# Optimization experiments

Hardware: AMD Instinct MI355X
Metric: run time of the kernel (lower is better)

Reference implementation:

```python
import jax, jax.numpy as jnp
import numpy as np

DIM = 384
RES = 32
NH = 8
RD = 2
B = 64


def _linear_params(key, out_f, in_f, scale=0.02, bias=True):
    kw, kb = jax.random.split(key)
    W = jax.random.normal(kw, (out_f, in_f), dtype=jnp.float32) * scale
    b = jax.random.normal(kb, (out_f,), dtype=jnp.float32) * scale if bias else None
    return W, b


def setup_inputs() -> dict:
    key = jax.random.key(0)
    ks = jax.random.split(key, 16)
    x = jax.random.normal(ks[0], (B, RES, RES, DIM), dtype=jnp.float32)
    Wc_h, bc_h = _linear_params(ks[1], NH * RD, DIM)
    Wg_h, bg_h = _linear_params(ks[2], RES * RES, RES * RD)
    Wo_h, bo_h = _linear_params(ks[3], DIM, DIM)
    Wc_w, bc_w = _linear_params(ks[4], NH * RD, DIM)
    Wg_w, bg_w = _linear_params(ks[5], RES * RES, RES * RD)
    Wo_w, bo_w = _linear_params(ks[6], DIM, DIM)
    Wmlpc, _ = _linear_params(ks[7], DIM, DIM, bias=False)
    Wr1, br1 = _linear_params(ks[8], DIM // 4, DIM)
    Wr2, br2 = _linear_params(ks[9], DIM * 3, DIM // 4)
    Wp, bp = _linear_params(ks[10], DIM, DIM)
    return dict(x=x, Wc_h=Wc_h, bc_h=bc_h, Wg_h=Wg_h, bg_h=bg_h, Wo_h=Wo_h, bo_h=bo_h,
                Wc_w=Wc_w, bc_w=bc_w, Wg_w=Wg_w, bg_w=bg_w, Wo_w=Wo_w, bo_w=bo_w,
                Wmlpc=Wmlpc, Wr1=Wr1, br1=br1, Wr2=Wr2, br2=br2, Wp=Wp, bp=bp)


def _dynamixer_op(x, Wc, bc, Wg, bg, Wo, bo):
    # x: [N, L, C]
    N, L, C = x.shape
    hd = C // NH
    # compress -> [N, L, NH*RD] -> [N, NH, L*RD]
    w = x @ Wc.T + bc
    w = w.reshape(N, L, NH, RD).transpose(0, 2, 1, 3).reshape(N, NH, L * RD)
    # generate -> [N, NH, L, L], softmax over axis -2 (rows)
    w = (w @ Wg.T + bg).reshape(N, NH, L, L)
    w = jax.nn.softmax(w, axis=-2)
    # x -> [N, NH, hd, L]; mix: y[n,h,d,j] = sum_l x[n,h,d,l] * w[n,h,l,j]
    xh = x.reshape(N, L, NH, hd).transpose(0, 2, 3, 1)
    y = jnp.einsum('nhdl,nhlj->nhdj', xh, w)
    y = y.transpose(0, 3, 1, 2).reshape(N, L, C)
    return y @ Wo.T + bo


def reference(x, Wc_h, bc_h, Wg_h, bg_h, Wo_h, bo_h,
              Wc_w, bc_w, Wg_w, bg_w, Wo_w, bo_w,
              Wmlpc, Wr1, br1, Wr2, br2, Wp, bp):
    Bn, H, W, C = x.shape
    # mix along H: batch over (B, W)
    h = _dynamixer_op(x.transpose(0, 2, 1, 3).reshape(Bn * W, H, C),
                      Wc_h, bc_h, Wg_h, bg_h, Wo_h, bo_h)
    h = h.reshape(Bn, W, H, C).transpose(0, 2, 1, 3)
    # mix along W: batch over (B, H)
    w = _dynamixer_op(x.reshape(Bn * H, W, C),
                      Wc_w, bc_w, Wg_w, bg_w, Wo_w, bo_w)
    w = w.reshape(Bn, H, W, C)
    # channel path (no bias)
    c = x @ Wmlpc.T
    # reweighting: global average pool over H, W
    a = (h + w + c).mean(axis=(1, 2))            # [B, C]
    a = jax.nn.gelu(a @ Wr1.T + br1, approximate=False) @ Wr2.T + br2  # [B, 3C]
    a = a.reshape(Bn, C, 3).transpose(2, 0, 1)   # [3, B, C]
    a = jax.nn.softmax(a, axis=0)[:, :, None, None, :]  # [3, B, 1, 1, C]
    out = h * a[0] + w * a[1] + c * a[2]
    return out @ Wp.T + bp
```

## Files before the change

### kernel.cpp

```cpp
#include <hip/hip_runtime.h>

typedef unsigned short u16;
typedef __bf16 bf16_t;
typedef bf16_t bf16x8 __attribute__((ext_vector_type(8)));
typedef float f32x4 __attribute__((ext_vector_type(4)));

__device__ __forceinline__ u16 f2b(float f) {
  union { float f; unsigned u; } v; v.f = f;
  unsigned r = (v.u + 0x7fffu + ((v.u >> 16) & 1u)) >> 16;
  return (u16)r;
}
__device__ __forceinline__ float b2f(u16 b) {
  union { unsigned u; float f; } v; v.u = ((unsigned)b) << 16;
  return v.f;
}
__device__ __forceinline__ f32x4 mfma16(bf16x8 a, bf16x8 b, f32x4 c) {
  return __builtin_amdgcn_mfma_f32_16x16x32_bf16(a, b, c, 0, 0, 0);
}

struct CvtJobs {
  const float* s[8];
  u16* d[8];
  int n[8];
};
__global__ void k0_cvt(CvtJobs j) {
  int job = blockIdx.y;
  const float* s = j.s[job];
  u16* d = j.d[job];
  int n = j.n[job];
  int stride = gridDim.x * blockDim.x * 4;
  for (int i = (blockIdx.x * blockDim.x + threadIdx.x) * 4; i < n; i += stride) {
    float4 v = *(const float4*)(s + i);
    ushort4 o4;
    o4.x = f2b(v.x); o4.y = f2b(v.y); o4.z = f2b(v.z); o4.w = f2b(v.w);
    *(ushort4*)(d + i) = o4;
  }
}

#define LW 392
#define TW 40
#define AW 40

__global__ __launch_bounds__(256, 2) void k1_mixer(
    const float* __restrict__ x,
    const u16* __restrict__ Wc_h_b, const float* __restrict__ bc_h,
    const u16* __restrict__ Wg_h_b, const float* __restrict__ bg_h,
    const u16* __restrict__ Wc_w_b, const float* __restrict__ bc_w,
    const u16* __restrict__ Wg_w_b, const float* __restrict__ bg_w,
    u16* __restrict__ y_h,
    float* __restrict__ psum_yh, float* __restrict__ psum_yw,
    float* __restrict__ psum_x)
{
  __shared__ u16 xs_b[32 * LW];
  __shared__ u16 xs_t[384 * TW];
  __shared__ u16 attn[8 * 32 * AW];
  __shared__ u16 whead[16 * 72];
  __shared__ float rs[8 * 32];

  const int tid = threadIdx.x;
  const int bid = blockIdx.x;
  const int path = bid >> 11;
  const int n = bid & 2047;
  const int b = n >> 5, o = n & 31;
  long base; int strideL;
  if (path == 0) { base = (long)b * 393216 + (long)o * 384;   strideL = 12288; }
  else           { base = (long)b * 393216 + (long)o * 12288; strideL = 384; }
  const float* xseq = x + base;

  const u16* Wc_b = path ? Wc_w_b : Wc_h_b;
  const float* bc = path ? bc_w : bc_h;
  const u16* Wg_b = path ? Wg_w_b : Wg_h_b;
  const float* bg = path ? bg_w : bg_h;

  for (int i = tid; i < 3072; i += 256) {
    int l = i / 96, c4 = (i % 96) * 4;
    float4 v = *(const float4*)(xseq + (long)l * strideL + c4);
    ushort4 w4;
    w4.x = f2b(v.x); w4.y = f2b(v.y); w4.z = f2b(v.z); w4.w = f2b(v.w);
    *(ushort4*)&xs_b[l * LW + c4] = w4;
  }
  for (int i = tid; i < 576; i += 256) whead[576 + i] = 0;
  __syncthreads();

  if (path == 0) {
    for (int i = tid; i < 3072; i += 256) {
      int c = i % 384, l4 = (i / 384) * 4;
      ushort4 w4;
      w4.x = xs_b[(l4 + 0) * LW + c];
      w4.y = xs_b[(l4 + 1) * LW + c];
      w4.z = xs_b[(l4 + 2) * LW + c];
      w4.w = xs_b[(l4 + 3) * LW + c];
      *(ushort4*)&xs_t[c * TW + l4] = w4;
    }
    for (int c = tid; c < 384; c += 256) {
      float s = 0.f;
      for (int l = 0; l < 32; l++) s += b2f(xs_b[l * LW + c]);
      psum_x[(long)n * 384 + c] = s;
    }
  }

  const int wave = tid >> 6, lane = tid & 63;
  const int lq = lane >> 4, lr = lane & 15;
  const f32x4 z = {0.f, 0.f, 0.f, 0.f};

  if (wave < 2) {
    f32x4 acc = z;
    for (int ks = 0; ks < 12; ks++) {
      bf16x8 af  = *(const bf16x8*)&xs_b[(wave * 16 + lr) * LW + ks * 32 + lq * 8];
      bf16x8 bfr = *(const bf16x8*)(Wc_b + lr * 384 + ks * 32 + lq * 8);
      acc = mfma16(af, bfr, acc);
    }
    float bcv = bc[lr];
    for (int r = 0; r < 4; r++) {
      int l = wave * 16 + lq * 4 + r;
      whead[(lr >> 1) * 72 + l * 2 + (lr & 1)] = f2b(acc[r] + bcv);
    }
  }
  __syncthreads();

  {
    bf16x8 ga0 = *(const bf16x8*)&whead[lr * 72 + lq * 8];
    bf16x8 ga1 = *(const bf16x8*)&whead[lr * 72 + 32 + lq * 8];
    for (int t = 0; t < 16; t++) {
      int nt = wave * 16 + t;
      const u16* wg = Wg_b + (nt * 16 + lr) * 64;
      bf16x8 gb0 = *(const bf16x8*)(wg + lq * 8);
      bf16x8 gb1 = *(const bf16x8*)(wg + 32 + lq * 8);
      f32x4 acc = z;
      acc = mfma16(ga0, gb0, acc);
      acc = mfma16(ga1, gb1, acc);
      if (lq < 2) {
        int m = nt * 16 + lr, ii = m >> 5, jj = m & 31;
        for (int r = 0; r < 4; r++)
          attn[((lq * 4 + r) * 32 + jj) * AW + ii] = f2b(acc[r]);
      }
    }
  }
  __syncthreads();

  {
    int h = tid >> 5, j = tid & 31;
    u16* row = &attn[(h * 32 + j) * AW];
    float v[32]; float mx = -1e30f;
    for (int i = 0; i < 32; i++) {
      v[i] = b2f(row[i]) + bg[i * 32 + j];
      mx = fmaxf(mx, v[i]);
    }
    float s = 0.f;
    for (int i = 0; i < 32; i++) { v[i] = __expf(v[i] - mx); s += v[i]; }
    float inv = 1.0f / s;
    for (int i = 0; i < 32; i++) row[i] = f2b(v[i] * inv);
  }
  __syncthreads();

  if (path == 0) {
    for (int hh = 0; hh < 2; hh++) {
      int h = wave * 2 + hh;
      bf16x8 bf0 = *(const bf16x8*)&attn[(h * 32 + lr) * AW + lq * 8];
      bf16x8 bf1 = *(const bf16x8*)&attn[(h * 32 + 16 + lr) * AW + lq * 8];
      for (int mt = 0; mt < 3; mt++) {
        bf16x8 af = *(const bf16x8*)&xs_t[(h * 48 + mt * 16 + lr) * TW + lq * 8];
        f32x4 a0 = mfma16(af, bf0, z);
        f32x4 a1 = mfma16(af, bf1, z);
        for (int r = 0; r < 4; r++) {
          int c = h * 48 + mt * 16 + lq * 4 + r;
          xs_b[lr * LW + c]        = f2b(a0[r]);
          xs_b[(16 + lr) * LW + c] = f2b(a1[r]);
        }
      }
    }
    __syncthreads();
    u16* yout = y_h + base;
    for (int i = tid; i < 1536; i += 256) {
      int l = i / 48, uu = (i % 48) * 8;
      *(uint4*)(yout + (long)l * strideL + uu) = *(const uint4*)&xs_b[l * LW + uu];
    }
    for (int c = tid; c < 384; c += 256) {
      float s = 0.f;
      for (int jj = 0; jj < 32; jj++) s += b2f(xs_b[jj * LW + c]);
      psum_yh[(long)n * 384 + c] = s;
    }
  } else {
    {
      int h = tid >> 5, l = tid & 31;
      float s = 0.f;
      for (int j = 0; j < 32; j++) s += b2f(attn[(h * 32 + j) * AW + l]);
      rs[h * 32 + l] = s;
    }
    __syncthreads();
    for (int c = tid; c < 384; c += 256) {
      int h = c / 48;
      float s = 0.f;
      for (int l = 0; l < 32; l++) s += b2f(xs_b[l * LW + c]) * rs[h * 32 + l];
      psum_yw[(long)n * 384 + c] = s;
    }
  }
}

__global__ __launch_bounds__(384) void k3_scales(
    const float* __restrict__ psum_yh, const float* __restrict__ psum_yw,
    const float* __restrict__ psum_x,
    const float* __restrict__ Wo_h, const float* __restrict__ bo_h,
    const float* __restrict__ Wo_w, const float* __restrict__ bo_w,
    const float* __restrict__ Wmlpc,
    const float* __restrict__ Wr1, const float* __restrict__ br1,
    const float* __restrict__ Wr2, const float* __restrict__ br2,
    float* __restrict__ scal)
{
  __shared__ float ph[384], pw[384], px[384], a[384], r1[96];
  int b = blockIdx.x, t = threadIdx.x;
  float sh = 0.f, sw = 0.f, sx = 0.f;
  for (int o = 0; o < 32; o++) {
    sh += psum_yh[(long)(b * 32 + o) * 384 + t];
    sw += psum_yw[(long)(b * 32 + o) * 384 + t];
    sx += psum_x[(long)(b * 32 + o) * 384 + t];
  }
  ph[t] = sh; pw[t] = sw; px[t] = sx;
  __syncthreads();
  float s1 = 0.f, s2 = 0.f, s3 = 0.f;
  for (int k = 0; k < 384; k++) {
    s1 += ph[k] * Wo_h[t * 384 + k];
    s2 += pw[k] * Wo_w[t * 384 + k];
    s3 += px[k] * Wmlpc[t * 384 + k];
  }
  a[t] = (s1 + s2 + s3) * (1.f / 1024.f) + bo_h[t] + bo_w[t];
  __syncthreads();
  if (t < 96) {
    float s = 0.f;
    for (int k = 0; k < 384; k++) s += a[k] * Wr1[t * 384 + k];
    s += br1[t];
    r1[t] = s * 0.5f * (1.f + erff(s * 0.70710678118654752f));
  }
  __syncthreads();
  {
    float sv[3];
    for (int si = 0; si < 3; si++) {
      float acc = 0.f;
      for (int k = 0; k < 96; k++) acc += r1[k] * Wr2[(t * 3 + si) * 96 + k];
      sv[si] = acc + br2[t * 3 + si];
    }
    float mx = fmaxf(sv[0], fmaxf(sv[1], sv[2]));
    float e0 = __expf(sv[0] - mx), e1 = __expf(sv[1] - mx), e2 = __expf(sv[2] - mx);
    float inv = 1.f / (e0 + e1 + e2);
    scal[0 * 24576 + b * 384 + t] = e0 * inv;
    scal[1 * 24576 + b * 384 + t] = e1 * inv;
    scal[2 * 24576 + b * 384 + t] = e2 * inv;
  }
}

__device__ __forceinline__ void gemm_regB(
    const u16* __restrict__ Bglob, const u16* __restrict__ bufA,
    f32x4 acc[4][6], int wm, int wn, int lq, int lr)
{
  const u16* bp0 = Bglob + (wn * 96 + lr) * 384 + lq * 8;
  const u16* ap0 = bufA + (wm * 64 + lr) * 392 + lq * 8;
  bf16x8 bcur[6], af[4];
#pragma unroll
  for (int nt = 0; nt < 6; nt++) bcur[nt] = *(const bf16x8*)(bp0 + nt * 6144);
#pragma unroll
  for (int mt = 0; mt < 4; mt++) af[mt] = *(const bf16x8*)(ap0 + mt * 6272);
  for (int ks = 0; ks < 12; ks++) {
    bf16x8 bnx[6], an[4];
    const int k1 = (ks < 11) ? (ks + 1) * 32 : 11 * 32;
#pragma unroll
    for (int nt = 0; nt < 6; nt++) bnx[nt] = *(const bf16x8*)(bp0 + nt * 6144 + k1);
#pragma unroll
    for (int mt = 0; mt < 4; mt++) an[mt] = *(const bf16x8*)(ap0 + mt * 6272 + k1);
#pragma unroll
    for (int nt = 0; nt < 6; nt++)
#pragma unroll
      for (int mt = 0; mt < 4; mt++)
        acc[mt][nt] = mfma16(af[mt], bcur[nt], acc[mt][nt]);
#pragma unroll
    for (int nt = 0; nt < 6; nt++) bcur[nt] = bnx[nt];
#pragma unroll
    for (int mt = 0; mt < 4; mt++) af[mt] = an[mt];
  }
}

__global__ __launch_bounds__(512, 2) void k24_final(
    const float* __restrict__ x, const u16* __restrict__ y_h,
    const u16* __restrict__ Wc_w_b, const float* __restrict__ bc_w,
    const u16* __restrict__ Wg_w_b, const float* __restrict__ bg_w,
    const u16* __restrict__ Wo_h_b, const u16* __restrict__ Wo_w_b,
    const u16* __restrict__ Wmlpc_b, const u16* __restrict__ Wp_b,
    const float* __restrict__ bo_h, const float* __restrict__ bo_w,
    const float* __restrict__ bp,
    const float* __restrict__ scal, float* __restrict__ out)
{
  __shared__ u16 bufA[128 * 392];
  __shared__ u16 Bs[384 * 40];
  __shared__ u16 attn[8 * 32 * AW];
  __shared__ u16 whead[16 * 72];

  const int tid = threadIdx.x;
  const int m0 = blockIdx.x * 128;
  const int b = m0 >> 10;
  const int wave = tid >> 6, lane = tid & 63;
  const int lq = lane >> 4, lr = lane & 15;
  const int wm = wave >> 2, wn = wave & 3;
  const f32x4 z = {0.f, 0.f, 0.f, 0.f};

  for (int i = tid; i < 12288; i += 512) {
    int row = i / 96, c4 = (i % 96) * 4;
    float4 v = *(const float4*)(x + (long)(m0 + row) * 384 + c4);
    ushort4 w4;
    w4.x = f2b(v.x); w4.y = f2b(v.y); w4.z = f2b(v.z); w4.w = f2b(v.w);
    *(ushort4*)&bufA[row * 392 + c4] = w4;
  }
  for (int i = tid; i < 576; i += 512) whead[576 + i] = 0;
  __syncthreads();

  f32x4 acc[4][6];
#pragma unroll
  for (int i = 0; i < 4; i++)
#pragma unroll
    for (int jn = 0; jn < 6; jn++) acc[i][jn] = z;

  gemm_regB(Wmlpc_b, bufA, acc, wm, wn, lq, lr);

  {
    const float* s2p = scal + 2 * 24576 + b * 384;
    const float* s1p = scal + 1 * 24576 + b * 384;
#pragma unroll
    for (int nt = 0; nt < 6; nt++) {
      int col = wn * 96 + nt * 16 + lr;
      float r = s2p[col] / fmaxf(s1p[col], 1e-30f);
#pragma unroll
      for (int mt = 0; mt < 4; mt++)
#pragma unroll
        for (int rr = 0; rr < 4; rr++) acc[mt][nt][rr] *= r;
    }
  }

  for (int q = 0; q < 4; q++) {
    for (int i = tid; i < 3072; i += 512) {
      int c = i % 384, l4 = (i / 384) * 4;
      ushort4 w4;
      w4.x = bufA[(q * 32 + l4 + 0) * 392 + c];
      w4.y = bufA[(q * 32 + l4 + 1) * 392 + c];
      w4.z = bufA[(q * 32 + l4 + 2) * 392 + c];
      w4.w = bufA[(q * 32 + l4 + 3) * 392 + c];
      *(ushort4*)&Bs[c * 40 + l4] = w4;
    }
    if (wave < 2) {
      f32x4 ac = z;
      for (int ks = 0; ks < 12; ks++) {
        bf16x8 afg = *(const bf16x8*)&bufA[(q * 32 + wave * 16 + lr) * 392 + ks * 32 + lq * 8];
        bf16x8 bfg = *(const bf16x8*)(Wc_w_b + lr * 384 + ks * 32 + lq * 8);
        ac = mfma16(afg, bfg, ac);
      }
      float bcv = bc_w[lr];
      for (int r = 0; r < 4; r++) {
        int l = wave * 16 + lq * 4 + r;
        whead[(lr >> 1) * 72 + l * 2 + (lr & 1)] = f2b(ac[r] + bcv);
      }
    }
    __syncthreads();
    {
      bf16x8 ga0 = *(const bf16x8*)&whead[lr * 72 + lq * 8];
      bf16x8 ga1 = *(const bf16x8*)&whead[lr * 72 + 32 + lq * 8];
      for (int t = 0; t < 8; t++) {
        int nt = wave * 8 + t;
        const u16* wg = Wg_w_b + (nt * 16 + lr) * 64;
        bf16x8 gb0 = *(const bf16x8*)(wg + lq * 8);
        bf16x8 gb1 = *(const bf16x8*)(wg + 32 + lq * 8);
        f32x4 ac = z;
        ac = mfma16(ga0, gb0, ac);
        ac = mfma16(ga1, gb1, ac);
        if (lq < 2) {
          int m = nt * 16 + lr, ii = m >> 5, jj = m & 31;
          for (int r = 0; r < 4; r++)
            attn[((lq * 4 + r) * 32 + jj) * AW + ii] = f2b(ac[r]);
        }
      }
    }
    __syncthreads();
    if (tid < 256) {
      int h = tid >> 5, j = tid & 31;
      u16* row = &attn[(h * 32 + j) * AW];
      float v[32]; float mx = -1e30f;
      for (int i = 0; i < 32; i++) {
        v[i] = b2f(row[i]) + bg_w[i * 32 + j];
        mx = fmaxf(mx, v[i]);
      }
      float s = 0.f;
      for (int i = 0; i < 32; i++) { v[i] = __expf(v[i] - mx); s += v[i]; }
      float inv = 1.0f / s;
      for (int i = 0; i < 32; i++) row[i] = f2b(v[i] * inv);
    }
    __syncthreads();
    {
      int h = wave;
      bf16x8 bf0 = *(const bf16x8*)&attn[(h * 32 + lr) * AW + lq * 8];
      bf16x8 bf1 = *(const bf16x8*)&attn[(h * 32 + 16 + lr) * AW + lq * 8];
      for (int mt = 0; mt < 3; mt++) {
        bf16x8 afg = *(const bf16x8*)&Bs[(h * 48 + mt * 16 + lr) * 40 + lq * 8];
        f32x4 a0 = mfma16(afg, bf0, z);
        f32x4 a1 = mfma16(afg, bf1, z);
        for (int r = 0; r < 4; r++) {
          int c = h * 48 + mt * 16 + lq * 4 + r;
          bufA[(q * 32 + lr) * 392 + c]      = f2b(a0[r]);
          bufA[(q * 32 + 16 + lr) * 392 + c] = f2b(a1[r]);
        }
      }
    }
    __syncthreads();
  }

  gemm_regB(Wo_w_b, bufA, acc, wm, wn, lq, lr);

  {
    const float* s1p = scal + 1 * 24576 + b * 384;
    const float* s0p = scal + 0 * 24576 + b * 384;
#pragma unroll
    for (int nt = 0; nt < 6; nt++) {
      int col = wn * 96 + nt * 16 + lr;
      float r = s1p[col] / fmaxf(s0p[col], 1e-30f);
#pragma unroll
      for (int mt = 0; mt < 4; mt++)
#pragma unroll
        for (int rr = 0; rr < 4; rr++) acc[mt][nt][rr] *= r;
    }
  }

  __syncthreads();

  for (int i = tid; i < 6144; i += 512) {
    int row = i / 48, u8 = (i % 48) * 8;
    *(uint4*)&bufA[row * 392 + u8] = *(const uint4*)(y_h + (long)(m0 + row) * 384 + u8);
  }
  __syncthreads();
  gemm_regB(Wo_h_b, bufA, acc, wm, wn, lq, lr);

  __syncthreads();

  {
    const float* s0p = scal + 0 * 24576 + b * 384;
    const float* s1p = scal + 1 * 24576 + b * 384;
#pragma unroll
    for (int nt = 0; nt < 6; nt++) {
      int col = wn * 96 + nt * 16 + lr;
      float s0v = s0p[col];
      float bcb = s0v * bo_h[col] + s1p[col] * bo_w[col];
#pragma unroll
      for (int mt = 0; mt < 4; mt++)
#pragma unroll
        for (int r = 0; r < 4; r++) {
          int row = wm * 64 + mt * 16 + lq * 4 + r;
          bufA[row * 392 + col] = f2b(acc[mt][nt][r] * s0v + bcb);
        }
    }
  }
  __syncthreads();

#pragma unroll
  for (int i = 0; i < 4; i++)
#pragma unroll
    for (int jn = 0; jn < 6; jn++) acc[i][jn] = z;
  gemm_regB(Wp_b, bufA, acc, wm, wn, lq, lr);
#pragma unroll
  for (int nt = 0; nt < 6; nt++) {
    int col = wn * 96 + nt * 16 + lr;
    float bi = bp[col];
#pragma unroll
    for (int mt = 0; mt < 4; mt++)
#pragma unroll
      for (int r = 0; r < 4; r++) {
        int row = m0 + wm * 64 + mt * 16 + lq * 4 + r;
        out[(long)row * 384 + col] = acc[mt][nt][r] + bi;
      }
  }
}

extern "C" void kernel_launch(void* const* d_in, const int* in_sizes, int n_in,
                              void* d_out, int out_size, void* d_ws, size_t ws_size,
                              hipStream_t stream) {
  const float* x     = (const float*)d_in[0];
  const float* Wc_h  = (const float*)d_in[1];
  const float* bc_h  = (const float*)d_in[2];
  const float* Wg_h  = (const float*)d_in[3];
  const float* bg_h  = (const float*)d_in[4];
  const float* Wo_h  = (const float*)d_in[5];
  const float* bo_h  = (const float*)d_in[6];
  const float* Wc_w  = (const float*)d_in[7];
  const float* bc_w  = (const float*)d_in[8];
  const float* Wg_w  = (const float*)d_in[9];
  const float* bg_w  = (const float*)d_in[10];
  const float* Wo_w  = (const float*)d_in[11];
  const float* bo_w  = (const float*)d_in[12];
  const float* Wmlpc = (const float*)d_in[13];
  const float* Wr1   = (const float*)d_in[14];
  const float* br1   = (const float*)d_in[15];
  const float* Wr2   = (const float*)d_in[16];
  const float* br2   = (const float*)d_in[17];
  const float* Wp    = (const float*)d_in[18];
  const float* bp    = (const float*)d_in[19];
  float* out = (float*)d_out;

  char* ws = (char*)d_ws;
  u16* y_h       = (u16*)(ws + 0);
  float* psum_yh = (float*)(ws + 50331648);
  float* psum_yw = (float*)(ws + 53477376);
  float* psum_x  = (float*)(ws + 56623104);
  float* scal    = (float*)(ws + 59768832);
  u16* Wc_h_b    = (u16*)(ws + 60063744);
  u16* Wc_w_b    = (u16*)(ws + 60076032);
  u16* Wg_h_b    = (u16*)(ws + 60088320);
  u16* Wg_w_b    = (u16*)(ws + 60219392);
  u16* Wo_h_b    = (u16*)(ws + 60350464);
  u16* Wo_w_b    = (u16*)(ws + 60645376);
  u16* Wmlpc_b   = (u16*)(ws + 60940288);
  u16* Wp_b      = (u16*)(ws + 61235200);

  CvtJobs jobs;
  jobs.s[0] = Wc_h;  jobs.d[0] = Wc_h_b;  jobs.n[0] = 6144;
  jobs.s[1] = Wc_w;  jobs.d[1] = Wc_w_b;  jobs.n[1] = 6144;
  jobs.s[2] = Wg_h;  jobs.d[2] = Wg_h_b;  jobs.n[2] = 65536;
  jobs.s[3] = Wg_w;  jobs.d[3] = Wg_w_b;  jobs.n[3] = 65536;
  jobs.s[4] = Wo_h;  jobs.d[4] = Wo_h_b;  jobs.n[4] = 147456;
  jobs.s[5] = Wo_w;  jobs.d[5] = Wo_w_b;  jobs.n[5] = 147456;
  jobs.s[6] = Wmlpc; jobs.d[6] = Wmlpc_b; jobs.n[6] = 147456;
  jobs.s[7] = Wp;    jobs.d[7] = Wp_b;    jobs.n[7] = 147456;
  k0_cvt<<<dim3(144, 8), 256, 0, stream>>>(jobs);

  k1_mixer<<<4096, 256, 0, stream>>>(x, Wc_h_b, bc_h, Wg_h_b, bg_h,
      Wc_w_b, bc_w, Wg_w_b, bg_w, y_h, psum_yh, psum_yw, psum_x);

  k3_scales<<<64, 384, 0, stream>>>(psum_yh, psum_yw, psum_x, Wo_h, bo_h,
      Wo_w, bo_w, Wmlpc, Wr1, br1, Wr2, br2, scal);

  k24_final<<<512, 512, 0, stream>>>(x, y_h, Wc_w_b, bc_w, Wg_w_b, bg_w,
      Wo_h_b, Wo_w_b, Wmlpc_b, Wp_b, bo_h, bo_w, bp, scal, out);
}
```

Before: 647.4 us.

## Materialize W-path mix output in k1 and drop recompute from final GEMM kernel

The W-axis mixer output is now computed once in k1_mixer, which writes it as bf16 into the output buffer (stride 768) and sums it directly for the pooling. The final kernel previously recomputed the whole W-path mixer (compress, generate, softmax, mix) per 128-row tile; now it just loads y_w. The final kernel is retiled to 64 rows per block with each wave covering 48 columns, which cuts shared memory and allows 6 blocks per CU. The cost is extra global write and read traffic for y_w. Reusing d_out as scratch is safe only because each block reads its own y_w rows before it writes out, and each 64-row block's bf16 stride-768 rows line up exactly with its own fp32 output rows.

After: 703.5 us. 8.7% more time.

```diff
diff --git a/kernel.cpp b/kernel.cpp
--- a/kernel.cpp
+++ b/kernel.cpp
@@ -47,7 +47,7 @@
     const u16* __restrict__ Wg_h_b, const float* __restrict__ bg_h,
     const u16* __restrict__ Wc_w_b, const float* __restrict__ bc_w,
     const u16* __restrict__ Wg_w_b, const float* __restrict__ bg_w,
-    u16* __restrict__ y_h,
+    u16* __restrict__ y_h, u16* y_w,
     float* __restrict__ psum_yh, float* __restrict__ psum_yw,
     float* __restrict__ psum_x)
 {
@@ -55,7 +55,6 @@
   __shared__ u16 xs_t[384 * TW];
   __shared__ u16 attn[8 * 32 * AW];
   __shared__ u16 whead[16 * 72];
-  __shared__ float rs[8 * 32];
 
   const int tid = threadIdx.x;
   const int bid = blockIdx.x;
@@ -82,16 +81,16 @@
   for (int i = tid; i < 576; i += 256) whead[576 + i] = 0;
   __syncthreads();
 
+  for (int i = tid; i < 3072; i += 256) {
+    int c = i % 384, l4 = (i / 384) * 4;
+    ushort4 w4;
+    w4.x = xs_b[(l4 + 0) * LW + c];
+    w4.y = xs_b[(l4 + 1) * LW + c];
+    w4.z = xs_b[(l4 + 2) * LW + c];
+    w4.w = xs_b[(l4 + 3) * LW + c];
+    *(ushort4*)&xs_t[c * TW + l4] = w4;
+  }
   if (path == 0) {
-    for (int i = tid; i < 3072; i += 256) {
-      int c = i % 384, l4 = (i / 384) * 4;
-      ushort4 w4;
-      w4.x = xs_b[(l4 + 0) * LW + c];
-      w4.y = xs_b[(l4 + 1) * LW + c];
-      w4.z = xs_b[(l4 + 2) * LW + c];
-      w4.w = xs_b[(l4 + 3) * LW + c];
-      *(ushort4*)&xs_t[c * TW + l4] = w4;
-    }
     for (int c = tid; c < 384; c += 256) {
       float s = 0.f;
       for (int l = 0; l < 32; l++) s += b2f(xs_b[l * LW + c]);
@@ -153,46 +152,42 @@
   }
   __syncthreads();
 
+  for (int hh = 0; hh < 2; hh++) {
+    int h = wave * 2 + hh;
+    bf16x8 bf0 = *(const bf16x8*)&attn[(h * 32 + lr) * AW + lq * 8];
+    bf16x8 bf1 = *(const bf16x8*)&attn[(h * 32 + 16 + lr) * AW + lq * 8];
+    for (int mt = 0; mt < 3; mt++) {
+      bf16x8 af = *(const bf16x8*)&xs_t[(h * 48 + mt * 16 + lr) * TW + lq * 8];
+      f32x4 a0 = mfma16(af, bf0, z);
+      f32x4 a1 = mfma16(af, bf1, z);
+      for (int r = 0; r < 4; r++) {
+        int c = h * 48 + mt * 16 + lq * 4 + r;
+        xs_b[lr * LW + c]        = f2b(a0[r]);
+        xs_b[(16 + lr) * LW + c] = f2b(a1[r]);
+      }
+    }
+  }
+  __syncthreads();
+
   if (path == 0) {
-    for (int hh = 0; hh < 2; hh++) {
-      int h = wave * 2 + hh;
-      bf16x8 bf0 = *(const bf16x8*)&attn[(h * 32 + lr) * AW + lq * 8];
-      bf16x8 bf1 = *(const bf16x8*)&attn[(h * 32 + 16 + lr) * AW + lq * 8];
-      for (int mt = 0; mt < 3; mt++) {
-        bf16x8 af = *(const bf16x8*)&xs_t[(h * 48 + mt * 16 + lr) * TW + lq * 8];
-        f32x4 a0 = mfma16(af, bf0, z);
-        f32x4 a1 = mfma16(af, bf1, z);
-        for (int r = 0; r < 4; r++) {
-          int c = h * 48 + mt * 16 + lq * 4 + r;
-          xs_b[lr * LW + c]        = f2b(a0[r]);
-          xs_b[(16 + lr) * LW + c] = f2b(a1[r]);
-        }
-      }
-    }
-    __syncthreads();
     u16* yout = y_h + base;
     for (int i = tid; i < 1536; i += 256) {
       int l = i / 48, uu = (i % 48) * 8;
-      *(uint4*)(yout + (long)l * strideL + uu) = *(const uint4*)&xs_b[l * LW + uu];
-    }
+      *(uint4*)(yout + (long)l * 12288 + uu) = *(const uint4*)&xs_b[l * LW + uu];
+    }
+  } else {
+    u16* yout = y_w + (long)(n * 32) * 768;
+    for (int i = tid; i < 1536; i += 256) {
+      int l = i / 48, uu = (i % 48) * 8;
+      *(uint4*)(yout + (long)l * 768 + uu) = *(const uint4*)&xs_b[l * LW + uu];
+    }
+  }
+  {
+    float* pdst = (path ? psum_yw : psum_yh) + (long)n * 384;
     for (int c = tid; c < 384; c += 256) {
       float s = 0.f;
       for (int jj = 0; jj < 32; jj++) s += b2f(xs_b[jj * LW + c]);
-      psum_yh[(long)n * 384 + c] = s;
-    }
-  } else {
-    {
-      int h = tid >> 5, l = tid & 31;
-      float s = 0.f;
-      for (int j = 0; j < 32; j++) s += b2f(attn[(h * 32 + j) * AW + l]);
-      rs[h * 32 + l] = s;
-    }
-    __syncthreads();
-    for (int c = tid; c < 384; c += 256) {
-      int h = c / 48;
-      float s = 0.f;
-      for (int l = 0; l < 32; l++) s += b2f(xs_b[l * LW + c]) * rs[h * 32 + l];
-      psum_yw[(long)n * 384 + c] = s;
+      pdst[c] = s;
     }
   }
 }
@@ -250,81 +245,74 @@
 
 __device__ __forceinline__ void gemm_regB(
     const u16* __restrict__ Bglob, const u16* __restrict__ bufA,
-    f32x4 acc[4][6], int wm, int wn, int lq, int lr)
+    f32x4 acc[4][3], int wn, int lq, int lr)
 {
-  const u16* bp0 = Bglob + (wn * 96 + lr) * 384 + lq * 8;
-  const u16* ap0 = bufA + (wm * 64 + lr) * 392 + lq * 8;
-  bf16x8 bcur[6], af[4];
-#pragma unroll
-  for (int nt = 0; nt < 6; nt++) bcur[nt] = *(const bf16x8*)(bp0 + nt * 6144);
+  const u16* bp0 = Bglob + (wn * 48 + lr) * 384 + lq * 8;
+  const u16* ap0 = bufA + lr * 392 + lq * 8;
+  bf16x8 bcur[3], af[4];
+#pragma unroll
+  for (int nt = 0; nt < 3; nt++) bcur[nt] = *(const bf16x8*)(bp0 + nt * 6144);
 #pragma unroll
   for (int mt = 0; mt < 4; mt++) af[mt] = *(const bf16x8*)(ap0 + mt * 6272);
   for (int ks = 0; ks < 12; ks++) {
-    bf16x8 bnx[6], an[4];
-    const int k1 = (ks < 11) ? (ks + 1) * 32 : 11 * 32;
-#pragma unroll
-    for (int nt = 0; nt < 6; nt++) bnx[nt] = *(const bf16x8*)(bp0 + nt * 6144 + k1);
+    bf16x8 bnx[3], an[4];
+    const int k1 = (ks < 11 ? ks + 1 : 11) * 32;
+#pragma unroll
+    for (int nt = 0; nt < 3; nt++) bnx[nt] = *(const bf16x8*)(bp0 + nt * 6144 + k1);
 #pragma unroll
     for (int mt = 0; mt < 4; mt++) an[mt] = *(const bf16x8*)(ap0 + mt * 6272 + k1);
 #pragma unroll
-    for (int nt = 0; nt < 6; nt++)
+    for (int nt = 0; nt < 3; nt++)
 #pragma unroll
       for (int mt = 0; mt < 4; mt++)
         acc[mt][nt] = mfma16(af[mt], bcur[nt], acc[mt][nt]);
 #pragma unroll
-    for (int nt = 0; nt < 6; nt++) bcur[nt] = bnx[nt];
+    for (int nt = 0; nt < 3; nt++) bcur[nt] = bnx[nt];
 #pragma unroll
     for (int mt = 0; mt < 4; mt++) af[mt] = an[mt];
   }
 }
 
-__global__ __launch_bounds__(512, 2) void k24_final(
-    const float* __restrict__ x, const u16* __restrict__ y_h,
-    const u16* __restrict__ Wc_w_b, const float* __restrict__ bc_w,
-    const u16* __restrict__ Wg_w_b, const float* __restrict__ bg_w,
+__global__ __launch_bounds__(512, 6) void k24_final(
+    const float* __restrict__ x, const u16* __restrict__ y_h, const u16* y_w,
     const u16* __restrict__ Wo_h_b, const u16* __restrict__ Wo_w_b,
     const u16* __restrict__ Wmlpc_b, const u16* __restrict__ Wp_b,
     const float* __restrict__ bo_h, const float* __restrict__ bo_w,
     const float* __restrict__ bp,
-    const float* __restrict__ scal, float* __restrict__ out)
+    const float* __restrict__ scal, float* out)
 {
-  __shared__ u16 bufA[128 * 392];
-  __shared__ u16 Bs[384 * 40];
-  __shared__ u16 attn[8 * 32 * AW];
-  __shared__ u16 whead[16 * 72];
+  __shared__ u16 bufA[64 * 392];
 
   const int tid = threadIdx.x;
-  const int m0 = blockIdx.x * 128;
+  const int m0 = blockIdx.x * 64;
   const int b = m0 >> 10;
   const int wave = tid >> 6, lane = tid & 63;
   const int lq = lane >> 4, lr = lane & 15;
-  const int wm = wave >> 2, wn = wave & 3;
+  const int wn = wave;
   const f32x4 z = {0.f, 0.f, 0.f, 0.f};
 
-  for (int i = tid; i < 12288; i += 512) {
+  for (int i = tid; i < 6144; i += 512) {
     int row = i / 96, c4 = (i % 96) * 4;
     float4 v = *(const float4*)(x + (long)(m0 + row) * 384 + c4);
     ushort4 w4;
     w4.x = f2b(v.x); w4.y = f2b(v.y); w4.z = f2b(v.z); w4.w = f2b(v.w);
     *(ushort4*)&bufA[row * 392 + c4] = w4;
   }
-  for (int i = tid; i < 576; i += 512) whead[576 + i] = 0;
-  __syncthreads();
-
-  f32x4 acc[4][6];
+  __syncthreads();
+
+  f32x4 acc[4][3];
 #pragma unroll
   for (int i = 0; i < 4; i++)
 #pragma unroll
-    for (int jn = 0; jn < 6; jn++) acc[i][jn] = z;
-
-  gemm_regB(Wmlpc_b, bufA, acc, wm, wn, lq, lr);
-
+    for (int jn = 0; jn < 3; jn++) acc[i][jn] = z;
+
+  gemm_regB(Wmlpc_b, bufA, acc, wn, lq, lr);
   {
     const float* s2p = scal + 2 * 24576 + b * 384;
     const float* s1p = scal + 1 * 24576 + b * 384;
 #pragma unroll
-    for (int nt = 0; nt < 6; nt++) {
-      int col = wn * 96 + nt * 16 + lr;
+    for (int nt = 0; nt < 3; nt++) {
+      int col = wn * 48 + nt * 16 + lr;
       float r = s2p[col] / fmaxf(s1p[col], 1e-30f);
 #pragma unroll
       for (int mt = 0; mt < 4; mt++)
@@ -332,90 +320,21 @@
         for (int rr = 0; rr < 4; rr++) acc[mt][nt][rr] *= r;
     }
   }
-
-  for (int q = 0; q < 4; q++) {
-    for (int i = tid; i < 3072; i += 512) {
-      int c = i % 384, l4 = (i / 384) * 4;
-      ushort4 w4;
-      w4.x = bufA[(q * 32 + l4 + 0) * 392 + c];
-      w4.y = bufA[(q * 32 + l4 + 1) * 392 + c];
-      w4.z = bufA[(q * 32 + l4 + 2) * 392 + c];
-      w4.w = bufA[(q * 32 + l4 + 3) * 392 + c];
-      *(ushort4*)&Bs[c * 40 + l4] = w4;
-    }
-    if (wave < 2) {
-      f32x4 ac = z;
-      for (int ks = 0; ks < 12; ks++) {
-        bf16x8 afg = *(const bf16x8*)&bufA[(q * 32 + wave * 16 + lr) * 392 + ks * 32 + lq * 8];
-        bf16x8 bfg = *(const bf16x8*)(Wc_w_b + lr * 384 + ks * 32 + lq * 8);
-        ac = mfma16(afg, bfg, ac);
-      }
-      float bcv = bc_w[lr];
-      for (int r = 0; r < 4; r++) {
-        int l = wave * 16 + lq * 4 + r;
-        whead[(lr >> 1) * 72 + l * 2 + (lr & 1)] = f2b(ac[r] + bcv);
-      }
-    }
-    __syncthreads();
-    {
-      bf16x8 ga0 = *(const bf16x8*)&whead[lr * 72 + lq * 8];
-      bf16x8 ga1 = *(const bf16x8*)&whead[lr * 72 + 32 + lq * 8];
-      for (int t = 0; t < 8; t++) {
-        int nt = wave * 8 + t;
-        const u16* wg = Wg_w_b + (nt * 16 + lr) * 64;
-        bf16x8 gb0 = *(const bf16x8*)(wg + lq * 8);
-        bf16x8 gb1 = *(const bf16x8*)(wg + 32 + lq * 8);
-        f32x4 ac = z;
-        ac = mfma16(ga0, gb0, ac);
-        ac = mfma16(ga1, gb1, ac);
-        if (lq < 2) {
-          int m = nt * 16 + lr, ii = m >> 5, jj = m & 31;
-          for (int r = 0; r < 4; r++)
-            attn[((lq * 4 + r) * 32 + jj) * AW + ii] = f2b(ac[r]);
-        }
-      }
-    }
-    __syncthreads();
-    if (tid < 256) {
-      int h = tid >> 5, j = tid & 31;
-      u16* row = &attn[(h * 32 + j) * AW];
-      float v[32]; float mx = -1e30f;
-      for (int i = 0; i < 32; i++) {
-        v[i] = b2f(row[i]) + bg_w[i * 32 + j];
-        mx = fmaxf(mx, v[i]);
-      }
-      float s = 0.f;
-      for (int i = 0; i < 32; i++) { v[i] = __expf(v[i] - mx); s += v[i]; }
-      float inv = 1.0f / s;
-      for (int i = 0; i < 32; i++) row[i] = f2b(v[i] * inv);
-    }
-    __syncthreads();
-    {
-      int h = wave;
-      bf16x8 bf0 = *(const bf16x8*)&attn[(h * 32 + lr) * AW + lq * 8];
-      bf16x8 bf1 = *(const bf16x8*)&attn[(h * 32 + 16 + lr) * AW + lq * 8];
-      for (int mt = 0; mt < 3; mt++) {
-        bf16x8 afg = *(const bf16x8*)&Bs[(h * 48 + mt * 16 + lr) * 40 + lq * 8];
-        f32x4 a0 = mfma16(afg, bf0, z);
-        f32x4 a1 = mfma16(afg, bf1, z);
-        for (int r = 0; r < 4; r++) {
-          int c = h * 48 + mt * 16 + lq * 4 + r;
-          bufA[(q * 32 + lr) * 392 + c]      = f2b(a0[r]);
-          bufA[(q * 32 + 16 + lr) * 392 + c] = f2b(a1[r]);
-        }
-      }
-    }
-    __syncthreads();
-  }
-
-  gemm_regB(Wo_w_b, bufA, acc, wm, wn, lq, lr);
-
+  __syncthreads();
+
+  for (int i = tid; i < 3072; i += 512) {
+    int row = i / 48, u8 = (i % 48) * 8;
+    *(uint4*)&bufA[row * 392 + u8] = *(const uint4*)(y_w + (long)(m0 + row) * 768 + u8);
+  }
+  __syncthreads();
+
+  gemm_regB(Wo_w_b, bufA, acc, wn, lq, lr);
   {
     const float* s1p = scal + 1 * 24576 + b * 384;
     const float* s0p = scal + 0 * 24576 + b * 384;
 #pragma unroll
-    for (int nt = 0; nt < 6; nt++) {
-      int col = wn * 96 + nt * 16 + lr;
+    for (int nt = 0; nt < 3; nt++) {
+      int col = wn * 48 + nt * 16 + lr;
       float r = s1p[col] / fmaxf(s0p[col], 1e-30f);
 #pragma unroll
       for (int mt = 0; mt < 4; mt++)
@@ -423,31 +342,30 @@
         for (int rr = 0; rr < 4; rr++) acc[mt][nt][rr] *= r;
     }
   }
-
-  __syncthreads();
-
-  for (int i = tid; i < 6144; i += 512) {
+  __syncthreads();
+
+  for (int i = tid; i < 3072; i += 512) {
     int row = i / 48, u8 = (i % 48) * 8;
     *(uint4*)&bufA[row * 392 + u8] = *(const uint4*)(y_h + (long)(m0 + row) * 384 + u8);
   }
   __syncthreads();
-  gemm_regB(Wo_h_b, bufA, acc, wm, wn, lq, lr);
-
+
+  gemm_regB(Wo_h_b, bufA, acc, wn, lq, lr);
   __syncthreads();
 
   {
     const float* s0p = scal + 0 * 24576 + b * 384;
     const float* s1p = scal + 1 * 24576 + b * 384;
 #pragma unroll
-    for (int nt = 0; nt < 6; nt++) {
-      int col = wn * 96 + nt * 16 + lr;
+    for (int nt = 0; nt < 3; nt++) {
+      int col = wn * 48 + nt * 16 + lr;
       float s0v = s0p[col];
       float bcb = s0v * bo_h[col] + s1p[col] * bo_w[col];
 #pragma unroll
       for (int mt = 0; mt < 4; mt++)
 #pragma unroll
         for (int r = 0; r < 4; r++) {
-          int row = wm * 64 + mt * 16 + lq * 4 + r;
+          int row = mt * 16 + lq * 4 + r;
           bufA[row * 392 + col] = f2b(acc[mt][nt][r] * s0v + bcb);
         }
     }
@@ -457,17 +375,17 @@
 #pragma unroll
   for (int i = 0; i < 4; i++)
 #pragma unroll
-    for (int jn = 0; jn < 6; jn++) acc[i][jn] = z;
-  gemm_regB(Wp_b, bufA, acc, wm, wn, lq, lr);
-#pragma unroll
-  for (int nt = 0; nt < 6; nt++) {
-    int col = wn * 96 + nt * 16 + lr;
+    for (int jn = 0; jn < 3; jn++) acc[i][jn] = z;
+  gemm_regB(Wp_b, bufA, acc, wn, lq, lr);
+#pragma unroll
+  for (int nt = 0; nt < 3; nt++) {
+    int col = wn * 48 + nt * 16 + lr;
     float bi = bp[col];
 #pragma unroll
     for (int mt = 0; mt < 4; mt++)
 #pragma unroll
       for (int r = 0; r < 4; r++) {
-        int row = m0 + wm * 64 + mt * 16 + lq * 4 + r;
+        int row = m0 + mt * 16 + lq * 4 + r;
         out[(long)row * 384 + col] = acc[mt][nt][r] + bi;
       }
   }
@@ -513,6 +431,8 @@
   u16* Wmlpc_b   = (u16*)(ws + 60940288);
   u16* Wp_b      = (u16*)(ws + 61235200);
 
+  u16* y_w = (u16*)d_out;
+
   CvtJobs jobs;
   jobs.s[0] = Wc_h;  jobs.d[0] = Wc_h_b;  jobs.n[0] = 6144;
   jobs.s[1] = Wc_w;  jobs.d[1] = Wc_w_b;  jobs.n[1] = 6144;
@@ -525,11 +445,11 @@
   k0_cvt<<<dim3(144, 8), 256, 0, stream>>>(jobs);
 
   k1_mixer<<<4096, 256, 0, stream>>>(x, Wc_h_b, bc_h, Wg_h_b, bg_h,
-      Wc_w_b, bc_w, Wg_w_b, bg_w, y_h, psum_yh, psum_yw, psum_x);
+      Wc_w_b, bc_w, Wg_w_b, bg_w, y_h, y_w, psum_yh, psum_yw, psum_x);
 
   k3_scales<<<64, 384, 0, stream>>>(psum_yh, psum_yw, psum_x, Wo_h, bo_h,
       Wo_w, bo_w, Wmlpc, Wr1, br1, Wr2, br2, scal);
 
-  k24_final<<<512, 512, 0, stream>>>(x, y_h, Wc_w_b, bc_w, Wg_w_b, bg_w,
+  k24_final<<<1024, 512, 0, stream>>>(x, y_h, y_w,
       Wo_h_b, Wo_w_b, Wmlpc_b, Wp_b, bo_h, bo_w, bp, scal, out);
 }
```

## Materialize W-path mixer output in k1 and use lighter 64-row final kernel

Applied to the files above, without the earlier changes.

When the workspace is large enough, k1_mixer now runs the full W-direction mix and writes y_w to global memory alongside y_h. A new final kernel uses 64-row tiles and simply streams y_w and y_h, so it no longer recomputes the W-path mixer. The old path is kept as a fallback and gains register prefetch of x and y_h ahead of the GEMMs. This removes redundant mixer compute in the final stage but adds a 50MB bf16 write and read, and depends on the harness workspace size.

Result: slower. 766.5 us (+18.4%).

```diff
diff --git a/kernel.cpp b/kernel.cpp
--- a/kernel.cpp
+++ b/kernel.cpp
@@ -47,7 +47,7 @@
     const u16* __restrict__ Wg_h_b, const float* __restrict__ bg_h,
     const u16* __restrict__ Wc_w_b, const float* __restrict__ bc_w,
     const u16* __restrict__ Wg_w_b, const float* __restrict__ bg_w,
-    u16* __restrict__ y_h,
+    u16* __restrict__ y_h, u16* __restrict__ y_w, int wmode,
     float* __restrict__ psum_yh, float* __restrict__ psum_yw,
     float* __restrict__ psum_x)
 {
@@ -71,6 +71,7 @@
   const float* bc = path ? bc_w : bc_h;
   const u16* Wg_b = path ? Wg_w_b : Wg_h_b;
   const float* bg = path ? bg_w : bg_h;
+  const int domix = (path == 0) || wmode;
 
   for (int i = tid; i < 3072; i += 256) {
     int l = i / 96, c4 = (i % 96) * 4;
@@ -82,7 +83,7 @@
   for (int i = tid; i < 576; i += 256) whead[576 + i] = 0;
   __syncthreads();
 
-  if (path == 0) {
+  if (domix) {
     for (int i = tid; i < 3072; i += 256) {
       int c = i % 384, l4 = (i / 384) * 4;
       ushort4 w4;
@@ -92,6 +93,8 @@
       w4.w = xs_b[(l4 + 3) * LW + c];
       *(ushort4*)&xs_t[c * TW + l4] = w4;
     }
+  }
+  if (path == 0) {
     for (int c = tid; c < 384; c += 256) {
       float s = 0.f;
       for (int l = 0; l < 32; l++) s += b2f(xs_b[l * LW + c]);
@@ -153,7 +156,7 @@
   }
   __syncthreads();
 
-  if (path == 0) {
+  if (domix) {
     for (int hh = 0; hh < 2; hh++) {
       int h = wave * 2 + hh;
       bf16x8 bf0 = *(const bf16x8*)&attn[(h * 32 + lr) * AW + lq * 8];
@@ -170,15 +173,24 @@
       }
     }
     __syncthreads();
-    u16* yout = y_h + base;
-    for (int i = tid; i < 1536; i += 256) {
-      int l = i / 48, uu = (i % 48) * 8;
-      *(uint4*)(yout + (long)l * strideL + uu) = *(const uint4*)&xs_b[l * LW + uu];
-    }
+    if (path == 0) {
+      u16* yout = y_h + base;
+      for (int i = tid; i < 1536; i += 256) {
+        int l = i / 48, uu = (i % 48) * 8;
+        *(uint4*)(yout + (long)l * 12288 + uu) = *(const uint4*)&xs_b[l * LW + uu];
+      }
+    } else {
+      u16* yout = y_w + (long)n * 12288;
+      for (int i = tid; i < 1536; i += 256) {
+        int l = i / 48, uu = (i % 48) * 8;
+        *(uint4*)(yout + (long)l * 384 + uu) = *(const uint4*)&xs_b[l * LW + uu];
+      }
+    }
+    float* pdst = (path ? psum_yw : psum_yh) + (long)n * 384;
     for (int c = tid; c < 384; c += 256) {
       float s = 0.f;
       for (int jj = 0; jj < 32; jj++) s += b2f(xs_b[jj * LW + c]);
-      psum_yh[(long)n * 384 + c] = s;
+      pdst[c] = s;
     }
   } else {
     {
@@ -248,7 +260,7 @@
   }
 }
 
-__device__ __forceinline__ void gemm_regB(
+__device__ __forceinline__ void gemm128(
     const u16* __restrict__ Bglob, const u16* __restrict__ bufA,
     f32x4 acc[4][6], int wm, int wn, int lq, int lr)
 {
@@ -261,7 +273,7 @@
   for (int mt = 0; mt < 4; mt++) af[mt] = *(const bf16x8*)(ap0 + mt * 6272);
   for (int ks = 0; ks < 12; ks++) {
     bf16x8 bnx[6], an[4];
-    const int k1 = (ks < 11) ? (ks + 1) * 32 : 11 * 32;
+    const int k1 = (ks < 11 ? ks + 1 : 11) * 32;
 #pragma unroll
     for (int nt = 0; nt < 6; nt++) bnx[nt] = *(const bf16x8*)(bp0 + nt * 6144 + k1);
 #pragma unroll
@@ -278,7 +290,37 @@
   }
 }
 
-__global__ __launch_bounds__(512, 2) void k24_final(
+__device__ __forceinline__ void gemm64(
+    const u16* __restrict__ Bglob, const u16* __restrict__ bufA,
+    f32x4 acc[2][6], int wm, int wn, int lq, int lr)
+{
+  const u16* bp0 = Bglob + (wn * 96 + lr) * 384 + lq * 8;
+  const u16* ap0 = bufA + (wm * 32 + lr) * 392 + lq * 8;
+  bf16x8 bcur[6], af[2];
+#pragma unroll
+  for (int nt = 0; nt < 6; nt++) bcur[nt] = *(const bf16x8*)(bp0 + nt * 6144);
+#pragma unroll
+  for (int mt = 0; mt < 2; mt++) af[mt] = *(const bf16x8*)(ap0 + mt * 6272);
+  for (int ks = 0; ks < 12; ks++) {
+    bf16x8 bnx[6], an[2];
+    const int k1 = (ks < 11 ? ks + 1 : 11) * 32;
+#pragma unroll
+    for (int nt = 0; nt < 6; nt++) bnx[nt] = *(const bf16x8*)(bp0 + nt * 6144 + k1);
+#pragma unroll
+    for (int mt = 0; mt < 2; mt++) an[mt] = *(const bf16x8*)(ap0 + mt * 6272 + k1);
+#pragma unroll
+    for (int nt = 0; nt < 6; nt++)
+#pragma unroll
+      for (int mt = 0; mt < 2; mt++)
+        acc[mt][nt] = mfma16(af[mt], bcur[nt], acc[mt][nt]);
+#pragma unroll
+    for (int nt = 0; nt < 6; nt++) bcur[nt] = bnx[nt];
+#pragma unroll
+    for (int mt = 0; mt < 2; mt++) af[mt] = an[mt];
+  }
+}
+
+__global__ __launch_bounds__(512, 2) void k24_final_B(
     const float* __restrict__ x, const u16* __restrict__ y_h,
     const u16* __restrict__ Wc_w_b, const float* __restrict__ bc_w,
     const u16* __restrict__ Wg_w_b, const float* __restrict__ bg_w,
@@ -301,12 +343,22 @@
   const int wm = wave >> 2, wn = wave & 3;
   const f32x4 z = {0.f, 0.f, 0.f, 0.f};
 
-  for (int i = tid; i < 12288; i += 512) {
-    int row = i / 96, c4 = (i % 96) * 4;
-    float4 v = *(const float4*)(x + (long)(m0 + row) * 384 + c4);
-    ushort4 w4;
-    w4.x = f2b(v.x); w4.y = f2b(v.y); w4.z = f2b(v.z); w4.w = f2b(v.w);
-    *(ushort4*)&bufA[row * 392 + c4] = w4;
+  for (int hb = 0; hb < 2; hb++) {
+    float4 xr[12];
+#pragma unroll
+    for (int j = 0; j < 12; j++) {
+      int i = hb * 6144 + j * 512 + tid;
+      int row = i / 96, c4 = (i % 96) * 4;
+      xr[j] = *(const float4*)(x + (long)(m0 + row) * 384 + c4);
+    }
+#pragma unroll
+    for (int j = 0; j < 12; j++) {
+      int i = hb * 6144 + j * 512 + tid;
+      int row = i / 96, c4 = (i % 96) * 4;
+      ushort4 w4;
+      w4.x = f2b(xr[j].x); w4.y = f2b(xr[j].y); w4.z = f2b(xr[j].z); w4.w = f2b(xr[j].w);
+      *(ushort4*)&bufA[row * 392 + c4] = w4;
+    }
   }
   for (int i = tid; i < 576; i += 512) whead[576 + i] = 0;
   __syncthreads();
@@ -317,8 +369,7 @@
 #pragma unroll
     for (int jn = 0; jn < 6; jn++) acc[i][jn] = z;
 
-  gemm_regB(Wmlpc_b, bufA, acc, wm, wn, lq, lr);
-
+  gemm128(Wmlpc_b, bufA, acc, wm, wn, lq, lr);
   {
     const float* s2p = scal + 2 * 24576 + b * 384;
     const float* s1p = scal + 1 * 24576 + b * 384;
@@ -408,8 +459,15 @@
     __syncthreads();
   }
 
-  gemm_regB(Wo_w_b, bufA, acc, wm, wn, lq, lr);
-
+  uint4 yh[12];
+#pragma unroll
+  for (int j = 0; j < 12; j++) {
+    int i = j * 512 + tid;
+    int row = i / 48, u8 = (i % 48) * 8;
+    yh[j] = *(const uint4*)(y_h + (long)(m0 + row) * 384 + u8);
+  }
+
+  gemm128(Wo_w_b, bufA, acc, wm, wn, lq, lr);
   {
     const float* s1p = scal + 1 * 24576 + b * 384;
     const float* s0p = scal + 0 * 24576 + b * 384;
@@ -423,16 +481,17 @@
         for (int rr = 0; rr < 4; rr++) acc[mt][nt][rr] *= r;
     }
   }
-
-  __syncthreads();
-
-  for (int i = tid; i < 6144; i += 512) {
+  __syncthreads();
+
+#pragma unroll
+  for (int j = 0; j < 12; j++) {
+    int i = j * 512 + tid;
     int row = i / 48, u8 = (i % 48) * 8;
-    *(uint4*)&bufA[row * 392 + u8] = *(const uint4*)(y_h + (long)(m0 + row) * 384 + u8);
-  }
-  __syncthreads();
-  gemm_regB(Wo_h_b, bufA, acc, wm, wn, lq, lr);
-
+    *(uint4*)&bufA[row * 392 + u8] = yh[j];
+  }
+  __syncthreads();
+
+  gemm128(Wo_h_b, bufA, acc, wm, wn, lq, lr);
   __syncthreads();
 
   {
@@ -458,7 +517,7 @@
   for (int i = 0; i < 4; i++)
 #pragma unroll
     for (int jn = 0; jn < 6; jn++) acc[i][jn] = z;
-  gemm_regB(Wp_b, bufA, acc, wm, wn, lq, lr);
+  gemm128(Wp_b, bufA, acc, wm, wn, lq, lr);
 #pragma unroll
   for (int nt = 0; nt < 6; nt++) {
     int col = wn * 96 + nt * 16 + lr;
@@ -468,6 +527,153 @@
 #pragma unroll
       for (int r = 0; r < 4; r++) {
         int row = m0 + wm * 64 + mt * 16 + lq * 4 + r;
+        out[(long)row * 384 + col] = acc[mt][nt][r] + bi;
+      }
+  }
+}
+
+__global__ __launch_bounds__(512, 2) void k24_final_A(
+    const float* __restrict__ x,
+    const u16* __restrict__ y_h, const u16* __restrict__ y_w,
+    const u16* __restrict__ Wo_h_b, const u16* __restrict__ Wo_w_b,
+    const u16* __restrict__ Wmlpc_b, const u16* __restrict__ Wp_b,
+    const float* __restrict__ bo_h, const float* __restrict__ bo_w,
+    const float* __restrict__ bp,
+    const float* __restrict__ scal, float* __restrict__ out)
+{
+  __shared__ u16 bufA[64 * 392];
+
+  const int tid = threadIdx.x;
+  const int m0 = blockIdx.x * 64;
+  const int b = m0 >> 10;
+  const int wave = tid >> 6, lane = tid & 63;
+  const int lq = lane >> 4, lr = lane & 15;
+  const int wm = wave >> 2, wn = wave & 3;
+  const f32x4 z = {0.f, 0.f, 0.f, 0.f};
+
+  {
+    float4 xr[12];
+#pragma unroll
+    for (int j = 0; j < 12; j++) {
+      int i = j * 512 + tid;
+      int row = i / 96, c4 = (i % 96) * 4;
+      xr[j] = *(const float4*)(x + (long)(m0 + row) * 384 + c4);
+    }
+#pragma unroll
+    for (int j = 0; j < 12; j++) {
+      int i = j * 512 + tid;
+      int row = i / 96, c4 = (i % 96) * 4;
+      ushort4 w4;
+      w4.x = f2b(xr[j].x); w4.y = f2b(xr[j].y); w4.z = f2b(xr[j].z); w4.w = f2b(xr[j].w);
+      *(ushort4*)&bufA[row * 392 + c4] = w4;
+    }
+  }
+  __syncthreads();
+
+  f32x4 acc[2][6];
+#pragma unroll
+  for (int i = 0; i < 2; i++)
+#pragma unroll
+    for (int jn = 0; jn < 6; jn++) acc[i][jn] = z;
+
+  uint4 ywr[6];
+#pragma unroll
+  for (int j = 0; j < 6; j++) {
+    int i = j * 512 + tid;
+    int row = i / 48, u8 = (i % 48) * 8;
+    ywr[j] = *(const uint4*)(y_w + (long)(m0 + row) * 384 + u8);
+  }
+
+  gemm64(Wmlpc_b, bufA, acc, wm, wn, lq, lr);
+  {
+    const float* s2p = scal + 2 * 24576 + b * 384;
+    const float* s1p = scal + 1 * 24576 + b * 384;
+#pragma unroll
+    for (int nt = 0; nt < 6; nt++) {
+      int col = wn * 96 + nt * 16 + lr;
+      float r = s2p[col] / fmaxf(s1p[col], 1e-30f);
+#pragma unroll
+      for (int mt = 0; mt < 2; mt++)
+#pragma unroll
+        for (int rr = 0; rr < 4; rr++) acc[mt][nt][rr] *= r;
+    }
+  }
+  __syncthreads();
+#pragma unroll
+  for (int j = 0; j < 6; j++) {
+    int i = j * 512 + tid;
+    int row = i / 48, u8 = (i % 48) * 8;
+    *(uint4*)&bufA[row * 392 + u8] = ywr[j];
+  }
+  __syncthreads();
+
+  uint4 yhr[6];
+#pragma unroll
+  for (int j = 0; j < 6; j++) {
+    int i = j * 512 + tid;
+    int row = i / 48, u8 = (i % 48) * 8;
+    yhr[j] = *(const uint4*)(y_h + (long)(m0 + row) * 384 + u8);
+  }
+
+  gemm64(Wo_w_b, bufA, acc, wm, wn, lq, lr);
+  {
+    const float* s1p = scal + 1 * 24576 + b * 384;
+    const float* s0p = scal + 0 * 24576 + b * 384;
+#pragma unroll
+    for (int nt = 0; nt < 6; nt++) {
+      int col = wn * 96 + nt * 16 + lr;
+      float r = s1p[col] / fmaxf(s0p[col], 1e-30f);
+#pragma unroll
+      for (int mt = 0; mt < 2; mt++)
+#pragma unroll
+        for (int rr = 0; rr < 4; rr++) acc[mt][nt][rr] *= r;
+    }
+  }
+  __syncthreads();
+#pragma unroll
+  for (int j = 0; j < 6; j++) {
+    int i = j * 512 + tid;
+    int row = i / 48, u8 = (i % 48) * 8;
+    *(uint4*)&bufA[row * 392 + u8] = yhr[j];
+  }
+  __syncthreads();
+
+  gemm64(Wo_h_b, bufA, acc, wm, wn, lq, lr);
+  __syncthreads();
+
+  {
+    const float* s0p = scal + 0 * 24576 + b * 384;
+    const float* s1p = scal + 1 * 24576 + b * 384;
+#pragma unroll
+    for (int nt = 0; nt < 6; nt++) {
+      int col = wn * 96 + nt * 16 + lr;
+      float s0v = s0p[col];
+      float bcb = s0v * bo_h[col] + s1p[col] * bo_w[col];
+#pragma unroll
+      for (int mt = 0; mt < 2; mt++)
+#pragma unroll
+        for (int r = 0; r < 4; r++) {
+          int row = wm * 32 + mt * 16 + lq * 4 + r;
+          bufA[row * 392 + col] = f2b(acc[mt][nt][r] * s0v + bcb);
+        }
+    }
+  }
+  __syncthreads();
+
+#pragma unroll
+  for (int i = 0; i < 2; i++)
+#pragma unroll
+    for (int jn = 0; jn < 6; jn++) acc[i][jn] = z;
+  gemm64(Wp_b, bufA, acc, wm, wn, lq, lr);
+#pragma unroll
+  for (int nt = 0; nt < 6; nt++) {
+    int col = wn * 96 + nt * 16 + lr;
+    float bi = bp[col];
+#pragma unroll
+    for (int mt = 0; mt < 2; mt++)
+#pragma unroll
+      for (int r = 0; r < 4; r++) {
+        int row = m0 + wm * 32 + mt * 16 + lq * 4 + r;
         out[(long)row * 384 + col] = acc[mt][nt][r] + bi;
       }
   }
@@ -513,6 +719,10 @@
   u16* Wmlpc_b   = (u16*)(ws + 60940288);
   u16* Wp_b      = (u16*)(ws + 61235200);
 
+  const size_t NEED_BIG = 61530112ULL + 50331648ULL;
+  int wmode = (ws_size >= NEED_BIG) ? 1 : 0;
+  u16* y_w = wmode ? (u16*)(ws + 61530112) : (u16*)(ws + 0) ;
+
   CvtJobs jobs;
   jobs.s[0] = Wc_h;  jobs.d[0] = Wc_h_b;  jobs.n[0] = 6144;
   jobs.s[1] = Wc_w;  jobs.d[1] = Wc_w_b;  jobs.n[1] = 6144;
@@ -525,11 +735,16 @@
   k0_cvt<<<dim3(144, 8), 256, 0, stream>>>(jobs);
 
   k1_mixer<<<4096, 256, 0, stream>>>(x, Wc_h_b, bc_h, Wg_h_b, bg_h,
-      Wc_w_b, bc_w, Wg_w_b, bg_w, y_h, psum_yh, psum_yw, psum_x);
+      Wc_w_b, bc_w, Wg_w_b, bg_w, y_h, y_w, wmode, psum_yh, psum_yw, psum_x);
 
   k3_scales<<<64, 384, 0, stream>>>(psum_yh, psum_yw, psum_x, Wo_h, bo_h,
       Wo_w, bo_w, Wmlpc, Wr1, br1, Wr2, br2, scal);
 
-  k24_final<<<512, 512, 0, stream>>>(x, y_h, Wc_w_b, bc_w, Wg_w_b, bg_w,
-      Wo_h_b, Wo_w_b, Wmlpc_b, Wp_b, bo_h, bo_w, bp, scal, out);
-}
+  if (wmode) {
+    k24_final_A<<<1024, 512, 0, stream>>>(x, y_h, y_w,
+        Wo_h_b, Wo_w_b, Wmlpc_b, Wp_b, bo_h, bo_w, bp, scal, out);
+  } else {
+    k24_final_B<<<512, 512, 0, stream>>>(x, y_h, Wc_w_b, bc_w, Wg_w_b, bg_w,
+        Wo_h_b, Wo_w_b, Wmlpc_b, Wp_b, bo_h, bo_w, bp, scal, out);
+  }
+}
```
